# Kernel optimization log

Hardware: AMD Instinct MI355X
Metric: run time of the kernel (lower is better)

## Reference

```python
import jax, jax.numpy as jnp
import numpy as np

K = 3        # kernel_size
STRIDE = 1
PAD = 1
DIL = 1


def setup_inputs() -> dict:
    key = jax.random.key(0)
    ks = jax.random.split(key, 5)
    B, C, H, W, O = 4, 64, 128, 128, 64
    x = jax.random.normal(ks[0], (B, C, H, W), jnp.float32)
    # small offset-conv weights -> offsets of a few pixels (realistic trained regime)
    offset_w = jax.random.normal(ks[1], (2 * K * K, C, K, K), jnp.float32) * 0.01
    offset_b = jax.random.normal(ks[2], (2 * K * K,), jnp.float32) * 0.01
    weight = jax.random.normal(ks[3], (O, C, K, K), jnp.float32)
    bias = jax.random.normal(ks[4], (O,), jnp.float32)
    return {"x": x, "offset_w": offset_w, "offset_b": offset_b,
            "weight": weight, "bias": bias}


def _conv2d(x, w, b):
    y = jax.lax.conv_general_dilated(
        x, w, window_strides=(STRIDE, STRIDE),
        padding=[(PAD, PAD), (PAD, PAD)],
        dimension_numbers=("NCHW", "OIHW", "NCHW"))
    return y + b[None, :, None, None]


def _deform_conv2d(x, offset, weight, bias):
    B, C, H, W = x.shape
    O = weight.shape[0]
    KK = K * K
    Ho, Wo = offset.shape[2], offset.shape[3]
    # offset channels ordered (y, x) per kernel tap: [B, KK, 2, Ho, Wo]
    off = offset.reshape(B, KK, 2, Ho, Wo)
    kyy, kxx = jnp.meshgrid(jnp.arange(K) * DIL, jnp.arange(K) * DIL, indexing="ij")
    kyy = kyy.reshape(KK).astype(x.dtype)
    kxx = kxx.reshape(KK).astype(x.dtype)
    base_y = (jnp.arange(Ho) * STRIDE - PAD).astype(x.dtype)
    base_x = (jnp.arange(Wo) * STRIDE - PAD).astype(x.dtype)
    # sampling positions [B, KK, Ho, Wo]
    py = base_y[None, None, :, None] + kyy[None, :, None, None] + off[:, :, 0]
    px = base_x[None, None, None, :] + kxx[None, :, None, None] + off[:, :, 1]

    y0 = jnp.floor(py); x0 = jnp.floor(px)
    y1 = y0 + 1.0;      x1 = x0 + 1.0
    wy1 = py - y0; wy0 = 1.0 - wy1
    wx1 = px - x0; wx0 = 1.0 - wx1

    xf = x.reshape(B, C, H * W)

    def corner(yc, xc):
        valid = (yc >= 0) & (yc < H) & (xc >= 0) & (xc < W)  # zero padding outside
        idx = (jnp.clip(yc, 0, H - 1) * W + jnp.clip(xc, 0, W - 1)).astype(jnp.int32)
        g = jax.vmap(lambda xb, ib: xb[:, ib.reshape(-1)])(xf, idx)  # [B, C, KK*Ho*Wo]
        g = g.reshape(B, C, KK, Ho, Wo)
        return g * valid[:, None].astype(x.dtype)

    val = (corner(y0, x0) * (wy0 * wx0)[:, None]
         + corner(y0, x1) * (wy0 * wx1)[:, None]
         + corner(y1, x0) * (wy1 * wx0)[:, None]
         + corner(y1, x1) * (wy1 * wx1)[:, None])  # [B, C, KK, Ho, Wo]

    out = jnp.einsum("bckhw,ock->bohw", val, weight.reshape(O, C, KK))
    return out + bias[None, :, None, None]


def reference(x, offset_w, offset_b, weight, bias):
    offset = _conv2d(x, offset_w, offset_b)
    return _deform_conv2d(x, offset, weight, bias)
```

## Files before the change

kernel.cpp:

```cpp
#include <hip/hip_runtime.h>

#define B_   4
#define C_   64
#define O_   64
#define H_   128
#define W_   128
#define HW_  (H_ * W_)
#define KK_  9
#define M_   18

typedef short  short8  __attribute__((ext_vector_type(8)));
typedef float  floatx4 __attribute__((ext_vector_type(4)));
typedef float  float2v __attribute__((ext_vector_type(2)));
typedef unsigned int   uint4v   __attribute__((ext_vector_type(4)));
typedef unsigned short ushort8v __attribute__((ext_vector_type(8)));

static __device__ __forceinline__ unsigned short f2bf(float f) {
    unsigned int u = __float_as_uint(f);
    u += 0x7FFFu + ((u >> 16) & 1u);
    return (unsigned short)(u >> 16);
}
static __device__ __forceinline__ float2v bf2x(unsigned int q) {
    float2v r;
    r.x = __uint_as_float(q << 16);
    r.y = __uint_as_float(q & 0xFFFF0000u);
    return r;
}
static __device__ __forceinline__ float2v pk_mul(float2v a, float2v b) {
    float2v d;
    asm("v_pk_mul_f32 %0, %1, %2" : "=v"(d) : "v"(a), "v"(b));
    return d;
}
static __device__ __forceinline__ float2v pk_fma(float2v a, float2v b, float2v c) {
    float2v d;
    asm("v_pk_fma_f32 %0, %1, %2, %3" : "=v"(d) : "v"(a), "v"(b), "v"(c));
    return d;
}

__global__ __launch_bounds__(256) void prep(
        const float* __restrict__ x, const float* __restrict__ w,
        const float* __restrict__ ow, unsigned short* __restrict__ xT,
        unsigned short* __restrict__ wtbf, unsigned short* __restrict__ owtbf) {
    const int blk = blockIdx.x;
    if (blk < 1024) {
        __shared__ unsigned short T[64][70];
        const int tid  = threadIdx.x;
        const int half = blk & 1;
        const int y    = (blk >> 1) & (H_ - 1);
        const int b    = blk >> 8;
        const float* xby = x + (size_t)b * C_ * HW_ + y * W_ + half * 64;
        for (int i = tid; i < 64 * 64; i += 256) {
            const int c = i >> 6, xc = i & 63;
            T[xc][c] = f2bf(xby[(size_t)c * HW_ + xc]);
        }
        __syncthreads();
        for (int j = tid; j < 512; j += 256) {
            const int x8 = j >> 3, c8 = j & 7;
            const int gq  = c8 >> 1;
            const int sub = (c8 & 1) * 8;
            uint4v pk;
            #pragma unroll
            for (int k = 0; k < 4; ++k)
                pk[k] = *(const unsigned int*)&T[x8][c8 * 8 + k * 2];
            unsigned short* dst = xT
                + ((size_t)(b * 4 + gq) * HW_ + y * W_ + half * 64 + x8) * 16
                + sub;
            *(uint4v*)dst = pk;
        }
    } else if (blk < 1042) {
        const int i = (blk - 1024) * 256 + threadIdx.x;
        const int lane = i & 63, rest = i >> 6;
        const int ot = rest & 3, cks = rest >> 2;
        const int chunk = cks / 6, ks = cks % 6;
        const int o = ot * 16 + (lane & 15);
        const int kbase = chunk * 192 + ks * 32 + (lane >> 4) * 8;
        ushort8v pk;
        #pragma unroll
        for (int j = 0; j < 8; ++j) {
            const int k = kbase + j;
            pk[j] = f2bf(w[o * 576 + (k & 63) * 9 + (k >> 6)]);
        }
        *(ushort8v*)&wtbf[(size_t)i * 8] = pk;
    } else {
        const int i = (blk - 1042) * 256 + threadIdx.x;
        const int lane = i & 63, rest = i >> 6;
        const int tile = rest & 1, tks = rest >> 1;
        const int tap = tks >> 1, ks = tks & 1;
        const int m = tile * 16 + (lane & 15);
        const int cb = ks * 32 + (lane >> 4) * 8;
        ushort8v pk;
        #pragma unroll
        for (int j = 0; j < 8; ++j)
            pk[j] = (m < M_) ? f2bf(ow[m * 576 + (cb + j) * 9 + tap])
                             : (unsigned short)0;
        *(ushort8v*)&owtbf[(size_t)i * 8] = pk;
    }
}

__global__ __launch_bounds__(512, 8) void dcn_fused(
        const unsigned short* __restrict__ xT,
        const unsigned short* __restrict__ owtbf, const float* __restrict__ ob,
        const unsigned short* __restrict__ wtbf, const float* __restrict__ bias,
        float* __restrict__ out) {
    __shared__ union {
        unsigned short P[3][66][72];
        float ep[4][64][17];
    } u;
    __shared__ float offs[4][M_][16];

    const int tid    = threadIdx.x;
    const int lane   = tid & 63;
    const int ws     = __builtin_amdgcn_readfirstlane(tid >> 6);
    const int p      = ws & 3;
    const int h      = ws >> 2;
    const int lane15 = lane & 15;
    const int quad   = lane >> 4;

    const int g    = blockIdx.x;
    const int xcd  = g & 7;
    const int slot = g >> 3;
    const int ho   = xcd * 16 + (slot >> 3);
    const int b    = (slot >> 1) & 3;
    const int wo_base = (slot & 1) << 6;

    const unsigned short* xTb = xT + (size_t)b * (4 * HW_ * 16);

    #pragma unroll
    for (int ky = 0; ky < 3; ++ky) {
        const int y  = ho - 1 + ky;
        const bool yv = (unsigned)y < (unsigned)H_;
        for (int j = tid; j < 66 * 8; j += 512) {
            const int r = j >> 3, c8 = j & 7;
            const int gq = c8 >> 1, sub = (c8 & 1) * 8;
            const int cx = wo_base + r - 1;
            ushort8v p0 = {0, 0, 0, 0, 0, 0, 0, 0};
            if (yv && (unsigned)cx < (unsigned)W_)
                p0 = *(const ushort8v*)&xTb[(size_t)gq * (HW_ * 16)
                                            + ((size_t)y * W_ + cx) * 16 + sub];
            *(ushort8v*)&u.P[ky][r][c8 * 8] = p0;
        }
    }
    __syncthreads();

    if (h == 0) {
        floatx4 oa0 = (floatx4){0.f, 0.f, 0.f, 0.f};
        floatx4 oa1 = (floatx4){0.f, 0.f, 0.f, 0.f};
        #pragma unroll
        for (int ky = 0; ky < 3; ++ky) {
            #pragma unroll
            for (int kx = 0; kx < 3; ++kx) {
                const int tap = ky * 3 + kx;
                #pragma unroll
                for (int ks = 0; ks < 2; ++ks) {
                    const int kk = ks * 32 + quad * 8;
                    const short8 af =
                        *(const short8*)&u.P[ky][p * 16 + lane15 + kx][kk];
                    const int fb = ((tap * 2 + ks) * 2) * 64 + lane;
                    const short8 bf0 = *(const short8*)&owtbf[(size_t)fb * 8];
                    const short8 bf1 =
                        *(const short8*)&owtbf[(size_t)(fb + 64) * 8];
                    oa0 = __builtin_amdgcn_mfma_f32_16x16x32_bf16(af, bf0, oa0, 0, 0, 0);
                    oa1 = __builtin_amdgcn_mfma_f32_16x16x32_bf16(af, bf1, oa1, 0, 0, 0);
                }
            }
        }
        const float ob0 = ob[lane15];
        #pragma unroll
        for (int r = 0; r < 4; ++r) oa0[r] += ob0;
        *(floatx4*)&offs[p][lane15][quad * 4] = oa0;
        if (lane15 < 2) {
            const float ob1 = ob[16 + lane15];
            #pragma unroll
            for (int r = 0; r < 4; ++r) oa1[r] += ob1;
            *(floatx4*)&offs[p][16 + lane15][quad * 4] = oa1;
        }
    }
    __syncthreads();

    const int pxg = p * 16 + lane15;
    floatx4 acc[4];
    #pragma unroll
    for (int t = 0; t < 4; ++t) acc[t] = (floatx4){0.f, 0.f, 0.f, 0.f};

    #pragma unroll 2
    for (int k = h; k < 9; k += 2) {
        const int ky = k / 3, kx = k - ky * 3;
        const float offy = offs[p][2 * k][lane15];
        const float offx = offs[p][2 * k + 1][lane15];
        const float py  = (float)(ho - 1 + ky) + offy;
        const float pxx = (float)(wo_base - 1 + kx + pxg) + offx;
        const float fy = floorf(py), fx = floorf(pxx);
        const int y0 = (int)fy, x0 = (int)fx;
        const int y1 = y0 + 1,  x1 = x0 + 1;
        const float wy1 = py - fy,  wy0 = 1.f - wy1;
        const float wx1 = pxx - fx, wx0 = 1.f - wx1;
        const bool y0v = (unsigned)y0 < (unsigned)H_;
        const bool y1v = (unsigned)y1 < (unsigned)H_;
        const bool x0v = (unsigned)x0 < (unsigned)W_;
        const bool x1v = (unsigned)x1 < (unsigned)W_;
        const float w00 = (y0v && x0v) ? wy0 * wx0 : 0.f;
        const float w01 = (y0v && x1v) ? wy0 * wx1 : 0.f;
        const float w10 = (y1v && x0v) ? wy1 * wx0 : 0.f;
        const float w11 = (y1v && x1v) ? wy1 * wx1 : 0.f;
        const float2v w00_2 = {w00, w00};
        const float2v w01_2 = {w01, w01};
        const float2v w10_2 = {w10, w10};
        const float2v w11_2 = {w11, w11};
        const int ry0 = min(max(y0, 0), H_ - 1);
        const int ry1 = min(max(y1, 0), H_ - 1);
        const int cx0 = min(max(x0, 0), W_ - 1);
        const int cx1 = min(max(x1, 0), W_ - 1);
        const int a00 = (ry0 * W_ + cx0) * 16;
        const int a01 = (ry0 * W_ + cx1) * 16;
        const int a10 = (ry1 * W_ + cx0) * 16;
        const int a11 = (ry1 * W_ + cx1) * 16;
        #pragma unroll
        for (int chalf = 0; chalf < 2; ++chalf) {
            const int c0 = chalf * 32 + quad * 8;
            const unsigned short* xp =
                xTb + (size_t)(c0 >> 4) * (HW_ * 16) + (c0 & 8);
            const uint4v q00 = *(const uint4v*)&xp[a00];
            const uint4v q01 = *(const uint4v*)&xp[a01];
            const uint4v q10 = *(const uint4v*)&xp[a10];
            const uint4v q11 = *(const uint4v*)&xp[a11];
            uint4v pw;
            #pragma unroll
            for (int j = 0; j < 4; ++j) {
                float2v v = pk_mul(bf2x(q00[j]), w00_2);
                v = pk_fma(bf2x(q01[j]), w01_2, v);
                v = pk_fma(bf2x(q10[j]), w10_2, v);
                v = pk_fma(bf2x(q11[j]), w11_2, v);
                pw[j] = __builtin_amdgcn_perm(
                    __float_as_uint(v.y) + 0x8000u,
                    __float_as_uint(v.x) + 0x8000u,
                    0x07060302u);
            }
            const short8 af = *(const short8*)&pw;
            const int cks = k * 2 + chalf;
            const unsigned short* wb = wtbf + (size_t)cks * 2048 + lane * 8;
            #pragma unroll
            for (int t = 0; t < 4; ++t) {
                const short8 bfrag = *(const short8*)&wb[(size_t)t * 512];
                acc[t] = __builtin_amdgcn_mfma_f32_16x16x32_bf16(
                             af, bfrag, acc[t], 0, 0, 0);
            }
        }
    }

    float* epw = &u.ep[p][0][0];
    if (h == 1) {
        #pragma unroll
        for (int t = 0; t < 4; ++t)
            #pragma unroll
            for (int r = 0; r < 4; ++r)
                epw[(t * 16 + lane15) * 17 + quad * 4 + r] = acc[t][r];
    }
    __syncthreads();
    if (h == 0) {
        #pragma unroll
        for (int t = 0; t < 4; ++t)
            #pragma unroll
            for (int r = 0; r < 4; ++r)
                epw[(t * 16 + lane15) * 17 + quad * 4 + r] += acc[t][r];
    }
    __syncthreads();

    const int wo = wo_base + p * 16 + lane15;
    #pragma unroll
    for (int i = 0; i < 8; ++i) {
        const int o = (h * 8 + i) * 4 + quad;
        out[(size_t)(b * O_ + o) * HW_ + ho * W_ + wo] =
            epw[o * 17 + lane15] + bias[o];
    }
}

extern "C" void kernel_launch(void* const* d_in, const int* in_sizes, int n_in,
                              void* d_out, int out_size, void* d_ws, size_t ws_size,
                              hipStream_t stream) {
    const float* x    = (const float*)d_in[0];
    const float* ow   = (const float*)d_in[1];
    const float* ob   = (const float*)d_in[2];
    const float* w    = (const float*)d_in[3];
    const float* bias = (const float*)d_in[4];
    float* out = (float*)d_out;

    unsigned short* wtbf  = (unsigned short*)d_ws;
    unsigned short* owtbf = wtbf + 4608 * 8;
    unsigned short* xT    = owtbf + 2304 * 8;

    prep<<<1051, 256, 0, stream>>>(x, w, ow, xT, wtbf, owtbf);
    dcn_fused<<<B_ * H_ * (W_ / 64), 512, 0, stream>>>(xT, owtbf, ob, wtbf, bias, out);
}
```

Before: 110.7 us.

## Stage 5-row swizzled input tile in LDS for offset conv and bilinear gathers

```diff
diff --git a/kernel.cpp b/kernel.cpp
--- a/kernel.cpp
+++ b/kernel.cpp
@@ -97,22 +97,22 @@
     }
 }
 
-__global__ __launch_bounds__(512, 8) void dcn_fused(
+__global__ __launch_bounds__(512, 6) void dcn_fused(
         const unsigned short* __restrict__ xT,
         const unsigned short* __restrict__ owtbf, const float* __restrict__ ob,
         const unsigned short* __restrict__ wtbf, const float* __restrict__ bias,
         float* __restrict__ out) {
+    __shared__ unsigned short tile[5][68][64];
     __shared__ union {
-        unsigned short P[3][66][72];
-        float ep[4][64][17];
-    } u;
-    __shared__ float offs[4][M_][16];
+        float offs[4][M_][16];
+        float mrg[2][4][16][17];
+    } v;
 
     const int tid    = threadIdx.x;
     const int lane   = tid & 63;
-    const int ws     = __builtin_amdgcn_readfirstlane(tid >> 6);
-    const int p      = ws & 3;
-    const int h      = ws >> 2;
+    const int wsl    = __builtin_amdgcn_readfirstlane(tid >> 6);
+    const int p      = wsl & 3;
+    const int h      = wsl >> 2;
     const int lane15 = lane & 15;
     const int quad   = lane >> 4;
 
@@ -124,27 +124,27 @@
     const int wo_base = (slot & 1) << 6;
 
     const unsigned short* xTb = xT + (size_t)b * (4 * HW_ * 16);
-
-    #pragma unroll
-    for (int ky = 0; ky < 3; ++ky) {
-        const int y  = ho - 1 + ky;
-        const bool yv = (unsigned)y < (unsigned)H_;
-        for (int j = tid; j < 66 * 8; j += 512) {
-            const int r = j >> 3, c8 = j & 7;
+    unsigned short* tp = &tile[0][0][0];
+
+    for (int j = tid; j < 5 * 68 * 8; j += 512) {
+        const int row = j / (68 * 8);
+        const int rem = j - row * (68 * 8);
+        const int px = rem >> 3, c8 = rem & 7;
+        const int y  = ho - 2 + row;
+        const int cx = wo_base - 2 + px;
+        ushort8v p0 = {0, 0, 0, 0, 0, 0, 0, 0};
+        if ((unsigned)y < (unsigned)H_ && (unsigned)cx < (unsigned)W_) {
             const int gq = c8 >> 1, sub = (c8 & 1) * 8;
-            const int cx = wo_base + r - 1;
-            ushort8v p0 = {0, 0, 0, 0, 0, 0, 0, 0};
-            if (yv && (unsigned)cx < (unsigned)W_)
-                p0 = *(const ushort8v*)&xTb[(size_t)gq * (HW_ * 16)
-                                            + ((size_t)y * W_ + cx) * 16 + sub];
-            *(ushort8v*)&u.P[ky][r][c8 * 8] = p0;
-        }
+            p0 = *(const ushort8v*)&xTb[(size_t)gq * (HW_ * 16)
+                                        + ((size_t)y * W_ + cx) * 16 + sub];
+        }
+        const int sl = c8 ^ (px & 7);
+        *(ushort8v*)&tp[(row * 68 + px) * 64 + sl * 8] = p0;
     }
     __syncthreads();
 
-    if (h == 0) {
-        floatx4 oa0 = (floatx4){0.f, 0.f, 0.f, 0.f};
-        floatx4 oa1 = (floatx4){0.f, 0.f, 0.f, 0.f};
+    {
+        floatx4 oa = (floatx4){0.f, 0.f, 0.f, 0.f};
         #pragma unroll
         for (int ky = 0; ky < 3; ++ky) {
             #pragma unroll
@@ -152,27 +152,26 @@
                 const int tap = ky * 3 + kx;
                 #pragma unroll
                 for (int ks = 0; ks < 2; ++ks) {
-                    const int kk = ks * 32 + quad * 8;
-                    const short8 af =
-                        *(const short8*)&u.P[ky][p * 16 + lane15 + kx][kk];
-                    const int fb = ((tap * 2 + ks) * 2) * 64 + lane;
-                    const short8 bf0 = *(const short8*)&owtbf[(size_t)fb * 8];
-                    const short8 bf1 =
-                        *(const short8*)&owtbf[(size_t)(fb + 64) * 8];
-                    oa0 = __builtin_amdgcn_mfma_f32_16x16x32_bf16(af, bf0, oa0, 0, 0, 0);
-                    oa1 = __builtin_amdgcn_mfma_f32_16x16x32_bf16(af, bf1, oa1, 0, 0, 0);
+                    const int pxA = p * 16 + lane15 + kx + 1;
+                    const int sA  = (ks * 4 + quad) ^ (pxA & 7);
+                    const short8 af = *(const short8*)
+                        &tp[((ky + 1) * 68 + pxA) * 64 + sA * 8];
+                    const int fb = ((tap * 2 + ks) * 2 + h) * 64 + lane;
+                    const short8 bf = *(const short8*)&owtbf[(size_t)fb * 8];
+                    oa = __builtin_amdgcn_mfma_f32_16x16x32_bf16(af, bf, oa, 0, 0, 0);
                 }
             }
         }
-        const float ob0 = ob[lane15];
-        #pragma unroll
-        for (int r = 0; r < 4; ++r) oa0[r] += ob0;
-        *(floatx4*)&offs[p][lane15][quad * 4] = oa0;
-        if (lane15 < 2) {
+        if (h == 0) {
+            const float ob0 = ob[lane15];
+            #pragma unroll
+            for (int r = 0; r < 4; ++r) oa[r] += ob0;
+            *(floatx4*)&v.offs[p][lane15][quad * 4] = oa;
+        } else if (lane15 < 2) {
             const float ob1 = ob[16 + lane15];
             #pragma unroll
-            for (int r = 0; r < 4; ++r) oa1[r] += ob1;
-            *(floatx4*)&offs[p][16 + lane15][quad * 4] = oa1;
+            for (int r = 0; r < 4; ++r) oa[r] += ob1;
+            *(floatx4*)&v.offs[p][16 + lane15][quad * 4] = oa;
         }
     }
     __syncthreads();
@@ -185,8 +184,8 @@
     #pragma unroll 2
     for (int k = h; k < 9; k += 2) {
         const int ky = k / 3, kx = k - ky * 3;
-        const float offy = offs[p][2 * k][lane15];
-        const float offx = offs[p][2 * k + 1][lane15];
+        const float offy = v.offs[p][2 * k][lane15];
+        const float offx = v.offs[p][2 * k + 1][lane15];
         const float py  = (float)(ho - 1 + ky) + offy;
         const float pxx = (float)(wo_base - 1 + kx + pxg) + offx;
         const float fy = floorf(py), fx = floorf(pxx);
@@ -210,29 +209,40 @@
         const int ry1 = min(max(y1, 0), H_ - 1);
         const int cx0 = min(max(x0, 0), W_ - 1);
         const int cx1 = min(max(x1, 0), W_ - 1);
-        const int a00 = (ry0 * W_ + cx0) * 16;
-        const int a01 = (ry0 * W_ + cx1) * 16;
-        const int a10 = (ry1 * W_ + cx0) * 16;
-        const int a11 = (ry1 * W_ + cx1) * 16;
+        const bool ok = (ry0 >= ho - 2) && (ry1 <= ho + 2) &&
+                        (cx0 >= wo_base - 2) && (cx1 <= wo_base + 65);
         #pragma unroll
         for (int chalf = 0; chalf < 2; ++chalf) {
-            const int c0 = chalf * 32 + quad * 8;
-            const unsigned short* xp =
-                xTb + (size_t)(c0 >> 4) * (HW_ * 16) + (c0 & 8);
-            const uint4v q00 = *(const uint4v*)&xp[a00];
-            const uint4v q01 = *(const uint4v*)&xp[a01];
-            const uint4v q10 = *(const uint4v*)&xp[a10];
-            const uint4v q11 = *(const uint4v*)&xp[a11];
+            const int c8 = chalf * 4 + quad;
+            uint4v q00, q01, q10, q11;
+            if (__all(ok)) {
+                const int r0 = (ry0 - (ho - 2)) * 68;
+                const int r1 = (ry1 - (ho - 2)) * 68;
+                const int p0 = cx0 - (wo_base - 2);
+                const int p1 = cx1 - (wo_base - 2);
+                q00 = *(const uint4v*)&tp[(r0 + p0) * 64 + ((c8 ^ (p0 & 7)) * 8)];
+                q01 = *(const uint4v*)&tp[(r0 + p1) * 64 + ((c8 ^ (p1 & 7)) * 8)];
+                q10 = *(const uint4v*)&tp[(r1 + p0) * 64 + ((c8 ^ (p0 & 7)) * 8)];
+                q11 = *(const uint4v*)&tp[(r1 + p1) * 64 + ((c8 ^ (p1 & 7)) * 8)];
+            } else {
+                const int c0 = chalf * 32 + quad * 8;
+                const unsigned short* xp =
+                    xTb + (size_t)(c0 >> 4) * (HW_ * 16) + (c0 & 8);
+                q00 = *(const uint4v*)&xp[(ry0 * W_ + cx0) * 16];
+                q01 = *(const uint4v*)&xp[(ry0 * W_ + cx1) * 16];
+                q10 = *(const uint4v*)&xp[(ry1 * W_ + cx0) * 16];
+                q11 = *(const uint4v*)&xp[(ry1 * W_ + cx1) * 16];
+            }
             uint4v pw;
             #pragma unroll
             for (int j = 0; j < 4; ++j) {
-                float2v v = pk_mul(bf2x(q00[j]), w00_2);
-                v = pk_fma(bf2x(q01[j]), w01_2, v);
-                v = pk_fma(bf2x(q10[j]), w10_2, v);
-                v = pk_fma(bf2x(q11[j]), w11_2, v);
+                float2v vv = pk_mul(bf2x(q00[j]), w00_2);
+                vv = pk_fma(bf2x(q01[j]), w01_2, vv);
+                vv = pk_fma(bf2x(q10[j]), w10_2, vv);
+                vv = pk_fma(bf2x(q11[j]), w11_2, vv);
                 pw[j] = __builtin_amdgcn_perm(
-                    __float_as_uint(v.y) + 0x8000u,
-                    __float_as_uint(v.x) + 0x8000u,
+                    __float_as_uint(vv.y) + 0x8000u,
+                    __float_as_uint(vv.x) + 0x8000u,
                     0x07060302u);
             }
             const short8 af = *(const short8*)&pw;
@@ -246,31 +256,43 @@
             }
         }
     }
-
-    float* epw = &u.ep[p][0][0];
-    if (h == 1) {
-        #pragma unroll
-        for (int t = 0; t < 4; ++t)
-            #pragma unroll
-            for (int r = 0; r < 4; ++r)
-                epw[(t * 16 + lane15) * 17 + quad * 4 + r] = acc[t][r];
-    }
     __syncthreads();
-    if (h == 0) {
-        #pragma unroll
-        for (int t = 0; t < 4; ++t)
-            #pragma unroll
-            for (int r = 0; r < 4; ++r)
-                epw[(t * 16 + lane15) * 17 + quad * 4 + r] += acc[t][r];
-    }
-    __syncthreads();
-
-    const int wo = wo_base + p * 16 + lane15;
+
     #pragma unroll
-    for (int i = 0; i < 8; ++i) {
-        const int o = (h * 8 + i) * 4 + quad;
-        out[(size_t)(b * O_ + o) * HW_ + ho * W_ + wo] =
-            epw[o * 17 + lane15] + bias[o];
+    for (int ph = 0; ph < 2; ++ph) {
+        if (h == 1) {
+            #pragma unroll
+            for (int tt = 0; tt < 2; ++tt)
+                #pragma unroll
+                for (int r = 0; r < 4; ++r)
+                    v.mrg[tt][p][lane15][quad * 4 + r] = acc[ph * 2 + tt][r];
+        }
+        __syncthreads();
+        if (h == 0) {
+            #pragma unroll
+            for (int tt = 0; tt < 2; ++tt) {
+                const float bs = bias[(ph * 2 + tt) * 16 + lane15];
+                #pragma unroll
+                for (int r = 0; r < 4; ++r)
+                    v.mrg[tt][p][lane15][quad * 4 + r] +=
+                        acc[ph * 2 + tt][r] + bs;
+            }
+        }
+        __syncthreads();
+        {
+            const int t2   = tid >> 8;
+            const int o16  = (tid >> 4) & 15;
+            const int px64 = (tid & 15) * 4;
+            const int pp   = px64 >> 4, wi = px64 & 15;
+            floatx4 val;
+            #pragma unroll
+            for (int kq = 0; kq < 4; ++kq)
+                val[kq] = v.mrg[t2][pp][o16][wi + kq];
+            const int o = (ph * 2 + t2) * 16 + o16;
+            *(floatx4*)&out[(size_t)(b * O_ + o) * HW_ + ho * W_ + wo_base + px64]
+                = val;
+        }
+        __syncthreads();
     }
 }
 
```

Measured after the change: 111.0 us. Within noise of the previous version (+0.3%).
